# Performance work log

Measured on AMD Instinct MI355X. Metric: run time of the kernel, lower is better.

The kernel has to match this reference:

```python
import jax, jax.numpy as jnp
import numpy as np

B, T, P, D, L = 16, 120, 96, 128, 2


def setup_inputs() -> dict:
    key = jax.random.key(0)
    k1, k2, k3, k4 = jax.random.split(key, 4)
    x = jax.random.normal(k1, (B, P, D, T), dtype=jnp.float32)
    # distances: symmetric-ish positive pairwise distances from random 3D points
    pts = jax.random.uniform(k2, (B, T, P, 3), dtype=jnp.float32) * 5.0
    diff = pts[:, :, :, None, :] - pts[:, :, None, :, :]
    distances = jnp.sqrt(jnp.sum(diff * diff, axis=-1) + 1e-12)
    # contiguous-prefix padding mask (matches the original self-loop loop semantics)
    counts = jax.random.randint(k3, (B,), P // 2, P + 1)
    padding_mask = jnp.arange(P)[None, :] < counts[:, None]
    # params: xavier_uniform with gain 1e-5 ~ tiny; bias 0; LN gamma=1, beta=0
    limit = 1e-5 * np.sqrt(6.0 / (D + D))
    W = jax.random.uniform(k4, (L, D, D), minval=-limit, maxval=limit, dtype=jnp.float32)
    b = jnp.zeros((L, D), dtype=jnp.float32)
    gamma = jnp.ones((L, D), dtype=jnp.float32)
    beta = jnp.zeros((L, D), dtype=jnp.float32)
    return {"x": x, "distances": distances, "padding_mask": padding_mask,
            "W": W, "b": b, "gamma": gamma, "beta": beta}


def _build_adjacency(distances, padding_mask):
    # valid_mask: [B,T,P,P]
    vm2d = (padding_mask[:, :, None] & padding_mask[:, None, :]).astype(distances.dtype)  # [B,P,P]
    vm = vm2d[:, None, :, :]
    vd = distances * vm
    pos = (vd > 0).astype(distances.dtype)
    n = jnp.sum(pos)
    mean = jnp.sum(vd * pos) / n
    var = jnp.sum(((vd - mean) ** 2) * pos) / (n - 1.0)  # unbiased, as torch.std
    sigma = jnp.sqrt(var) + 1e-8
    adj = jnp.exp(-(distances ** 2) / (2.0 * sigma ** 2)) * vm
    # self loops on valid (contiguous-prefix) nodes: add diag(mask)
    eye_mask = jnp.eye(P, dtype=distances.dtype)[None, :, :] * padding_mask[:, :, None].astype(distances.dtype)
    adj = adj + eye_mask[:, None, :, :]
    # symmetric normalization D^{-1/2} A D^{-1/2}
    deg = jnp.clip(jnp.sum(adj, axis=-1, keepdims=True), 1e-8, None)  # [B,T,P,1]
    deg = jnp.clip(deg * padding_mask[:, None, :, None].astype(distances.dtype), 1e-8, None)
    dis = deg ** -0.5
    adj = dis * adj * jnp.swapaxes(dis, -2, -1)
    return adj * vm


def _layer_norm_D(x, g, bt, eps=1e-5):
    # x: [B,P,D,T]; normalize over D axis
    mu = jnp.mean(x, axis=2, keepdims=True)
    var = jnp.mean((x - mu) ** 2, axis=2, keepdims=True)
    return (x - mu) * jax.lax.rsqrt(var + eps) * g[None, None, :, None] + bt[None, None, :, None]


def reference(x, distances, padding_mask, W, b, gamma, beta):
    adj = _build_adjacency(distances, padding_mask)  # [B,T,P,P]
    mask_f = padding_mask.astype(x.dtype)
    for l in range(L):
        xt = jnp.transpose(x, (0, 3, 1, 2))                      # [B,T,P,D]
        h = jnp.einsum('btpd,de->btpe', xt, W[l])                # x @ W
        o = jnp.einsum('btpq,btqd->btpd', adj, h)                # A @ xW
        o = jax.nn.relu(o + b[l])
        o = o * mask_f[:, None, :, None]
        o = jnp.transpose(o, (0, 2, 3, 1))                       # [B,P,D,T]
        o = _layer_norm_D(o, gamma[l], beta[l])
        x = x + o
    return x
```

## Files before the change

### kernel.cpp

```cpp
#include <hip/hip_runtime.h>
#include <math.h>

typedef __bf16 bf16_t;
typedef __bf16 bf16x8 __attribute__((ext_vector_type(8)));
typedef __bf16 bf16x4 __attribute__((ext_vector_type(4)));
typedef float f32x4 __attribute__((ext_vector_type(4)));

namespace {
constexpr int kB = 16;
constexpr int kT = 120;
constexpr int kP = 96;
constexpr int kD = 128;
constexpr int kBT = kB * kT;
constexpr int kPP = kP * kP;
constexpr int kPD = kP * kD;
constexpr long long kND = (long long)kBT * kPP;

constexpr int YS = 136;
constexpr int HS = 104;
constexpr int OS = 132;
constexpr int AS = 104;
constexpr int UNION_B = 26624;
constexpr int AL_OFF = UNION_B;
constexpr int MROW_OFF = AL_OFF + 19968;
constexpr int SMEM_B = MROW_OFF + 384;
}

__device__ __forceinline__ f32x4 mfma16(bf16x8 a, bf16x8 b, f32x4 c) {
    return __builtin_amdgcn_mfma_f32_16x16x32_bf16(a, b, c, 0, 0, 0);
}

__global__ void k_mask(const unsigned char* __restrict__ mraw, int* __restrict__ mask,
                       double* __restrict__ stats) {
    int tid = threadIdx.x;
    if (tid < 4) stats[tid] = 0.0;
    const unsigned int* u32 = (const unsigned int*)mraw;
    unsigned int w0 = u32[0];
    int mode;
    if (w0 == 0x01010101u) mode = 0;
    else if (w0 == 1u) mode = 1;
    else mode = 2;
    for (int i = tid; i < kB * kP; i += blockDim.x) {
        int v;
        if (mode == 0)      v = (mraw[i] != 0);
        else if (mode == 1) v = (u32[i] != 0);
        else                v = (((const float*)mraw)[i] != 0.0f);
        mask[i] = v;
    }
}

__global__ void k_prep(const float* __restrict__ W, bf16_t* __restrict__ wT) {
    int l = blockIdx.y;
    int idx = blockIdx.x * 256 + threadIdx.x;
    int n = idx >> 7, k = idx & 127;
    wT[l * 16384 + n * 128 + k] = (bf16_t)W[l * 16384 + k * 128 + n];
}

__global__ __launch_bounds__(256) void k_stats(const float* __restrict__ dist,
                                               const int* __restrict__ mask,
                                               double* __restrict__ stats) {
    __shared__ int ml[kB * kP];
    for (int i = threadIdx.x; i < kB * kP; i += 256) ml[i] = mask[i];
    __syncthreads();

    long long n4 = kND / 4;
    long long stride = (long long)gridDim.x * 256;
    double s = 0.0, s2 = 0.0;
    int cnt = 0;
    for (long long i4 = (long long)blockIdx.x * 256 + threadIdx.x; i4 < n4; i4 += stride) {
        int q0 = 4 * (int)(i4 % 24);
        long long r = i4 / 24;
        int p = (int)(r % 96);
        int b = (int)((r / 96) / kT);
        const int* mb = ml + b * kP;
        if (mb[p]) {
            float4 d4 = *(const float4*)(dist + i4 * 4);
            if (mb[q0 + 0]) { s += d4.x; s2 += (double)d4.x * d4.x; cnt++; }
            if (mb[q0 + 1]) { s += d4.y; s2 += (double)d4.y * d4.y; cnt++; }
            if (mb[q0 + 2]) { s += d4.z; s2 += (double)d4.z * d4.z; cnt++; }
            if (mb[q0 + 3]) { s += d4.w; s2 += (double)d4.w * d4.w; cnt++; }
        }
    }
    __shared__ double sh[256];
    int tid = threadIdx.x;
    sh[tid] = s; __syncthreads();
    for (int off = 128; off > 0; off >>= 1) { if (tid < off) sh[tid] += sh[tid + off]; __syncthreads(); }
    if (tid == 0) atomicAdd(&stats[0], sh[0]);
    __syncthreads();
    sh[tid] = s2; __syncthreads();
    for (int off = 128; off > 0; off >>= 1) { if (tid < off) sh[tid] += sh[tid + off]; __syncthreads(); }
    if (tid == 0) atomicAdd(&stats[1], sh[0]);
    __syncthreads();
    sh[tid] = (double)cnt; __syncthreads();
    for (int off = 128; off > 0; off >>= 1) { if (tid < off) sh[tid] += sh[tid + off]; __syncthreads(); }
    if (tid == 0) atomicAdd(&stats[2], sh[0]);
}

__global__ void k_fin(const double* __restrict__ stats, float* __restrict__ params) {
    double n = stats[2];
    double mean = stats[0] / n;
    double var = (stats[1] - n * mean * mean) / (n - 1.0);
    double sigma = sqrt(var) + 1e-8;
    params[0] = (float)(1.0 / (2.0 * sigma * sigma));
}

__global__ __launch_bounds__(256) void k_adj(const float* __restrict__ dist,
                                             const int* __restrict__ mask,
                                             const float* __restrict__ params,
                                             bf16_t* __restrict__ adj) {
    __shared__ float aT[kP * 100];
    __shared__ float dis[kP];
    __shared__ float mr[kP];
    int bt = blockIdx.x;
    int b = bt / kT;
    int tid = threadIdx.x;
    if (tid < kP) mr[tid] = (float)mask[b * kP + tid];
    float inv2s2 = params[0];
    __syncthreads();
    const float* dbt = dist + (long long)bt * kPP;
    #pragma unroll
    for (int k = 0; k < 9; ++k) {
        int i4 = k * 256 + tid;
        int e = i4 * 4;
        int p = e / kP, q = e - p * kP;
        float4 d4 = *(const float4*)(dbt + e);
        float mp = mr[p];
        float v[4];
        v[0] = mp * mr[q + 0] != 0.f ? __expf(-d4.x * d4.x * inv2s2) : 0.f;
        v[1] = mp * mr[q + 1] != 0.f ? __expf(-d4.y * d4.y * inv2s2) : 0.f;
        v[2] = mp * mr[q + 2] != 0.f ? __expf(-d4.z * d4.z * inv2s2) : 0.f;
        v[3] = mp * mr[q + 3] != 0.f ? __expf(-d4.w * d4.w * inv2s2) : 0.f;
        #pragma unroll
        for (int j = 0; j < 4; ++j) {
            if (p == q + j) v[j] += mp;
            aT[p * 100 + q + j] = v[j];
        }
    }
    __syncthreads();
    if (tid < kP) {
        float s = 0.f;
        for (int q = 0; q < kP; ++q) s += aT[q * 100 + tid];
        s = fmaxf(s, 1e-8f);
        s = fmaxf(s * mr[tid], 1e-8f);
        dis[tid] = rsqrtf(s);
    }
    __syncthreads();
    bf16_t* obt = adj + (long long)bt * kPP;
    #pragma unroll
    for (int k = 0; k < 9; ++k) {
        int i4 = k * 256 + tid;
        int e = i4 * 4;
        int p = e / kP, q = e - p * kP;
        float dp = dis[p];
        bf16x4 ov;
        #pragma unroll
        for (int j = 0; j < 4; ++j)
            ov[j] = (bf16_t)(dp * aT[p * 100 + q + j] * dis[q + j]);
        *(bf16x4*)(obt + e) = ov;
    }
}

__global__ __launch_bounds__(256) void k_tin(const float* __restrict__ x,
                                             bf16_t* __restrict__ y) {
    __shared__ float tile[64 * 121];
    int b = blockIdx.y, pd0 = blockIdx.x * 64;
    int tid = threadIdx.x;
    const float* xb = x + ((long long)b * kPD + pd0) * kT;
    #pragma unroll
    for (int k = 0; k < 8; ++k) {
        int idx = k * 256 + tid;
        if (idx < 1920) {
            int r = idx / 30, c = idx - r * 30;
            float4 v = *(const float4*)(xb + r * kT + c * 4);
            tile[r * 121 + c * 4 + 0] = v.x;
            tile[r * 121 + c * 4 + 1] = v.y;
            tile[r * 121 + c * 4 + 2] = v.z;
            tile[r * 121 + c * 4 + 3] = v.w;
        }
    }
    __syncthreads();
    bf16_t* yb = y + (long long)b * kT * kPD + pd0;
    #pragma unroll
    for (int k = 0; k < 4; ++k) {
        int idx = k * 256 + tid;
        if (idx < 960) {
            int t = idx >> 3, dg = idx & 7;
            bf16x8 o;
            #pragma unroll
            for (int j = 0; j < 8; ++j) o[j] = (bf16_t)tile[(dg * 8 + j) * 121 + t];
            *(bf16x8*)(yb + (long long)t * kPD + dg * 8) = o;
        }
    }
}

__global__ __launch_bounds__(256) void k_tout(const bf16_t* __restrict__ y,
                                              float* __restrict__ out) {
    __shared__ float tile[64 * 121];
    int b = blockIdx.y, pd0 = blockIdx.x * 64;
    int tid = threadIdx.x;
    const bf16_t* yb = y + (long long)b * kT * kPD + pd0;
    #pragma unroll
    for (int k = 0; k < 4; ++k) {
        int idx = k * 256 + tid;
        if (idx < 960) {
            int t = idx >> 3, dg = idx & 7;
            bf16x8 v = *(const bf16x8*)(yb + (long long)t * kPD + dg * 8);
            #pragma unroll
            for (int j = 0; j < 8; ++j) tile[(dg * 8 + j) * 121 + t] = (float)v[j];
        }
    }
    __syncthreads();
    float* ob = out + ((long long)b * kPD + pd0) * kT;
    #pragma unroll
    for (int k = 0; k < 8; ++k) {
        int idx = k * 256 + tid;
        if (idx < 1920) {
            int r = idx / 30, c = idx - r * 30;
            float4 v;
            v.x = tile[r * 121 + c * 4 + 0];
            v.y = tile[r * 121 + c * 4 + 1];
            v.z = tile[r * 121 + c * 4 + 2];
            v.w = tile[r * 121 + c * 4 + 3];
            *(float4*)(ob + r * kT + c * 4) = v;
        }
    }
}

__global__ __launch_bounds__(512, 5) void k_gcn(bf16_t* __restrict__ y,
                                                const bf16_t* __restrict__ adj,
                                                const int* __restrict__ mask,
                                                const bf16_t* __restrict__ wT,
                                                const float* __restrict__ bias,
                                                const float* __restrict__ gamma,
                                                const float* __restrict__ beta) {
    __shared__ __align__(16) char smem[SMEM_B];
    bf16_t* yL  = (bf16_t*)smem;
    bf16_t* hT  = (bf16_t*)smem;
    bf16_t* oLb = (bf16_t*)smem;
    bf16_t* aL  = (bf16_t*)(smem + AL_OFF);
    float* mrowf = (float*)(smem + MROW_OFF);

    const int tid = threadIdx.x;
    const int tx = tid & 15, ty = tid >> 4;
    const int lane = tid & 63, w = tid >> 6;
    const int wm = w >> 2, wn = w & 3;
    const int fc = lane & 15, fg = lane >> 4;
    const int bt = blockIdx.x, b = bt / kT;
    const int d0 = tx * 8;

    bf16_t* ybt = y + (size_t)bt * kPD;
    const bf16_t* abt = adj + (size_t)bt * kPP;

    if (tid < kP) mrowf[tid] = (float)mask[b * kP + tid];

    #pragma unroll
    for (int k = 0; k < 5; ++k) {
        int i4 = k * 512 + tid;
        if (i4 < 2304) {
            int e4 = i4 * 4;
            int p = e4 / kP, q = e4 - p * kP;
            *(bf16x4*)(aL + p * AS + q) = *(const bf16x4*)(abt + e4);
        }
    }

    bf16x8 yR[3];
    #pragma unroll
    for (int i = 0; i < 3; ++i) {
        int p = ty * 3 + i;
        yR[i] = *(const bf16x8*)(ybt + p * kD + d0);
        *(bf16x8*)(yL + p * YS + d0) = yR[i];
    }

    for (int l = 0; l < 2; ++l) {
        const bf16_t* wTl = wT + l * kD * kD;
        bf16x8 wf[4][2];
        #pragma unroll
        for (int kt = 0; kt < 4; ++kt) {
            wf[kt][0] = *(const bf16x8*)(wTl + ((wn * 2 + 0) * 16 + fc) * kD + kt * 32 + fg * 8);
            wf[kt][1] = *(const bf16x8*)(wTl + ((wn * 2 + 1) * 16 + fc) * kD + kt * 32 + fg * 8);
        }
        __syncthreads();

        f32x4 acc[3][2];
        #pragma unroll
        for (int mt = 0; mt < 3; ++mt) { acc[mt][0] = {0,0,0,0}; acc[mt][1] = {0,0,0,0}; }
        #pragma unroll
        for (int kt = 0; kt < 4; ++kt) {
            #pragma unroll
            for (int mt = 0; mt < 3; ++mt) {
                bf16x8 af = *(const bf16x8*)(yL + ((wm * 3 + mt) * 16 + fc) * YS + kt * 32 + fg * 8);
                acc[mt][0] = mfma16(af, wf[kt][0], acc[mt][0]);
                acc[mt][1] = mfma16(af, wf[kt][1], acc[mt][1]);
            }
        }
        __syncthreads();

        #pragma unroll
        for (int mt = 0; mt < 3; ++mt)
            #pragma unroll
            for (int nn = 0; nn < 2; ++nn) {
                int e = (wn * 2 + nn) * 16 + fc;
                int p0 = (wm * 3 + mt) * 16 + fg * 4;
                bf16x4 hv = {(bf16_t)acc[mt][nn][0], (bf16_t)acc[mt][nn][1],
                             (bf16_t)acc[mt][nn][2], (bf16_t)acc[mt][nn][3]};
                *(bf16x4*)(hT + e * HS + p0) = hv;
            }
        __syncthreads();

        f32x4 acc2[3][2];
        #pragma unroll
        for (int mt = 0; mt < 3; ++mt) { acc2[mt][0] = {0,0,0,0}; acc2[mt][1] = {0,0,0,0}; }
        #pragma unroll
        for (int kt = 0; kt < 3; ++kt) {
            bf16x8 bf0 = *(const bf16x8*)(hT + ((wn * 2 + 0) * 16 + fc) * HS + kt * 32 + fg * 8);
            bf16x8 bf1 = *(const bf16x8*)(hT + ((wn * 2 + 1) * 16 + fc) * HS + kt * 32 + fg * 8);
            #pragma unroll
            for (int mt = 0; mt < 3; ++mt) {
                bf16x8 af = *(const bf16x8*)(aL + ((wm * 3 + mt) * 16 + fc) * AS + kt * 32 + fg * 8);
                acc2[mt][0] = mfma16(af, bf0, acc2[mt][0]);
                acc2[mt][1] = mfma16(af, bf1, acc2[mt][1]);
            }
        }
        __syncthreads();

        #pragma unroll
        for (int mt = 0; mt < 3; ++mt)
            #pragma unroll
            for (int nn = 0; nn < 2; ++nn) {
                int d = (wn * 2 + nn) * 16 + fc;
                int p0 = (wm * 3 + mt) * 16 + fg * 4;
                oLb[(p0 + 0) * OS + d] = (bf16_t)acc2[mt][nn][0];
                oLb[(p0 + 1) * OS + d] = (bf16_t)acc2[mt][nn][1];
                oLb[(p0 + 2) * OS + d] = (bf16_t)acc2[mt][nn][2];
                oLb[(p0 + 3) * OS + d] = (bf16_t)acc2[mt][nn][3];
            }
        __syncthreads();

        const float* bl = bias + l * kD;
        const float* gl = gamma + l * kD;
        const float* bel = beta + l * kD;
        float4 bb0 = *(const float4*)(bl + d0), bb1 = *(const float4*)(bl + d0 + 4);
        float4 gg0 = *(const float4*)(gl + d0), gg1 = *(const float4*)(gl + d0 + 4);
        float4 be0 = *(const float4*)(bel + d0), be1 = *(const float4*)(bel + d0 + 4);
        float bb[8] = {bb0.x, bb0.y, bb0.z, bb0.w, bb1.x, bb1.y, bb1.z, bb1.w};
        float gg[8] = {gg0.x, gg0.y, gg0.z, gg0.w, gg1.x, gg1.y, gg1.z, gg1.w};
        float be[8] = {be0.x, be0.y, be0.z, be0.w, be1.x, be1.y, be1.z, be1.w};

        #pragma unroll
        for (int i = 0; i < 3; ++i) {
            int p = ty * 3 + i;
            float mpf = mrowf[p];
            bf16x4 o0 = *(const bf16x4*)(oLb + p * OS + d0);
            bf16x4 o1 = *(const bf16x4*)(oLb + p * OS + d0 + 4);
            float v[8];
            #pragma unroll
            for (int j = 0; j < 4; ++j) {
                v[j]     = fmaxf((float)o0[j] + bb[j], 0.f) * mpf;
                v[j + 4] = fmaxf((float)o1[j] + bb[j + 4], 0.f) * mpf;
            }
            float s = v[0] + v[1] + v[2] + v[3] + v[4] + v[5] + v[6] + v[7];
            s += __shfl_xor(s, 8);
            s += __shfl_xor(s, 4);
            s += __shfl_xor(s, 2);
            s += __shfl_xor(s, 1);
            float mu = s * 0.0078125f;

            float ss = 0.f;
            #pragma unroll
            for (int j = 0; j < 8; ++j) { float dv = v[j] - mu; ss += dv * dv; }
            ss += __shfl_xor(ss, 8);
            ss += __shfl_xor(ss, 4);
            ss += __shfl_xor(ss, 2);
            ss += __shfl_xor(ss, 1);
            float inv = rsqrtf(ss * 0.0078125f + 1e-5f);

            bf16x8 c;
            #pragma unroll
            for (int j = 0; j < 8; ++j)
                c[j] = (bf16_t)((float)yR[i][j] + (v[j] - mu) * inv * gg[j] + be[j]);
            yR[i] = c;
        }

        if (l == 0) {
            __syncthreads();
            #pragma unroll
            for (int i = 0; i < 3; ++i)
                *(bf16x8*)(yL + (ty * 3 + i) * YS + d0) = yR[i];
        } else {
            #pragma unroll
            for (int i = 0; i < 3; ++i)
                *(bf16x8*)(ybt + (ty * 3 + i) * kD + d0) = yR[i];
        }
    }
}

extern "C" void kernel_launch(void* const* d_in, const int* in_sizes, int n_in,
                              void* d_out, int out_size, void* d_ws, size_t ws_size,
                              hipStream_t stream) {
    (void)in_sizes; (void)n_in; (void)out_size; (void)ws_size;

    const float* x = (const float*)d_in[0];
    const float* dist = (const float*)d_in[1];
    const unsigned char* mraw = (const unsigned char*)d_in[2];
    const float* W = (const float*)d_in[3];
    const float* bias = (const float*)d_in[4];
    const float* gamma = (const float*)d_in[5];
    const float* beta = (const float*)d_in[6];
    float* out = (float*)d_out;

    char* ws = (char*)d_ws;
    double* stats = (double*)ws;
    float* params = (float*)(ws + 32);
    int* mask = (int*)(ws + 64);
    bf16_t* wT = (bf16_t*)(ws + 8192);
    bf16_t* adj = (bf16_t*)(ws + 81920);
    bf16_t* y = (bf16_t*)(ws + 81920 + (size_t)kBT * kPP * 2);

    k_mask<<<1, 256, 0, stream>>>(mraw, mask, stats);
    k_prep<<<dim3(64, 2), 256, 0, stream>>>(W, wT);
    k_stats<<<1024, 256, 0, stream>>>(dist, mask, stats);
    k_fin<<<1, 1, 0, stream>>>(stats, params);
    k_adj<<<kBT, 256, 0, stream>>>(dist, mask, params, adj);

    k_tin<<<dim3(kPD / 64, kB), 256, 0, stream>>>(x, y);

    k_gcn<<<kBT, 512, 0, stream>>>(y, adj, mask, wT, bias, gamma, beta);

    k_tout<<<dim3(kPD / 64, kB), 256, 0, stream>>>(y, out);
}
```

Before: 212.3 us.

## Fuse adjacency construction into GCN kernel and merge mask/prep launches

Adjacency normalization is now computed inside the GCN kernel from raw distances. This removes the bf16 adjacency write and re-read through global memory, along with the separate k_adj and k_fin launches. The mask kernel is merged into the weight-transpose kernel to cut another launch, and y is kept in LDS rather than registers. In exchange, shared memory grows to about 73KB and the launch bounds drop to 2 blocks per CU, which lowers occupancy and adds the exp and normalization work to the GCN critical path.

```diff
diff --git a/kernel.cpp b/kernel.cpp
--- a/kernel.cpp
+++ b/kernel.cpp
@@ -20,40 +20,43 @@
 constexpr int HS = 104;
 constexpr int OS = 132;
 constexpr int AS = 104;
-constexpr int UNION_B = 26624;
-constexpr int AL_OFF = UNION_B;
-constexpr int MROW_OFF = AL_OFF + 19968;
-constexpr int SMEM_B = MROW_OFF + 384;
+constexpr int HT_OFF = 26112;
+constexpr int AL_OFF = 52736;
+constexpr int MROW_OFF = 72704;
+constexpr int DIS_OFF = 73088;
+constexpr int SMEM_B = 73472;
 }
 
 __device__ __forceinline__ f32x4 mfma16(bf16x8 a, bf16x8 b, f32x4 c) {
     return __builtin_amdgcn_mfma_f32_16x16x32_bf16(a, b, c, 0, 0, 0);
 }
 
-__global__ void k_mask(const unsigned char* __restrict__ mraw, int* __restrict__ mask,
+__global__ void k_prep(const float* __restrict__ W, bf16_t* __restrict__ wT,
+                       const unsigned char* __restrict__ mraw, int* __restrict__ mask,
                        double* __restrict__ stats) {
-    int tid = threadIdx.x;
-    if (tid < 4) stats[tid] = 0.0;
-    const unsigned int* u32 = (const unsigned int*)mraw;
-    unsigned int w0 = u32[0];
-    int mode;
-    if (w0 == 0x01010101u) mode = 0;
-    else if (w0 == 1u) mode = 1;
-    else mode = 2;
-    for (int i = tid; i < kB * kP; i += blockDim.x) {
-        int v;
-        if (mode == 0)      v = (mraw[i] != 0);
-        else if (mode == 1) v = (u32[i] != 0);
-        else                v = (((const float*)mraw)[i] != 0.0f);
-        mask[i] = v;
-    }
-}
-
-__global__ void k_prep(const float* __restrict__ W, bf16_t* __restrict__ wT) {
-    int l = blockIdx.y;
-    int idx = blockIdx.x * 256 + threadIdx.x;
+    int bid = blockIdx.x;
+    int l = bid >> 6;
+    int idx = (bid & 63) * 256 + threadIdx.x;
     int n = idx >> 7, k = idx & 127;
     wT[l * 16384 + n * 128 + k] = (bf16_t)W[l * 16384 + k * 128 + n];
+
+    if (bid == 0) {
+        int tid = threadIdx.x;
+        if (tid < 4) stats[tid] = 0.0;
+        const unsigned int* u32 = (const unsigned int*)mraw;
+        unsigned int w0 = u32[0];
+        int mode;
+        if (w0 == 0x01010101u) mode = 0;
+        else if (w0 == 1u) mode = 1;
+        else mode = 2;
+        for (int i = tid; i < kB * kP; i += 256) {
+            int v;
+            if (mode == 0)      v = (mraw[i] != 0);
+            else if (mode == 1) v = (u32[i] != 0);
+            else                v = (((const float*)mraw)[i] != 0.0f);
+            mask[i] = v;
+        }
+    }
 }
 
 __global__ __launch_bounds__(256) void k_stats(const float* __restrict__ dist,
@@ -96,70 +99,6 @@
     if (tid == 0) atomicAdd(&stats[2], sh[0]);
 }
 
-__global__ void k_fin(const double* __restrict__ stats, float* __restrict__ params) {
-    double n = stats[2];
-    double mean = stats[0] / n;
-    double var = (stats[1] - n * mean * mean) / (n - 1.0);
-    double sigma = sqrt(var) + 1e-8;
-    params[0] = (float)(1.0 / (2.0 * sigma * sigma));
-}
-
-__global__ __launch_bounds__(256) void k_adj(const float* __restrict__ dist,
-                                             const int* __restrict__ mask,
-                                             const float* __restrict__ params,
-                                             bf16_t* __restrict__ adj) {
-    __shared__ float aT[kP * 100];
-    __shared__ float dis[kP];
-    __shared__ float mr[kP];
-    int bt = blockIdx.x;
-    int b = bt / kT;
-    int tid = threadIdx.x;
-    if (tid < kP) mr[tid] = (float)mask[b * kP + tid];
-    float inv2s2 = params[0];
-    __syncthreads();
-    const float* dbt = dist + (long long)bt * kPP;
-    #pragma unroll
-    for (int k = 0; k < 9; ++k) {
-        int i4 = k * 256 + tid;
-        int e = i4 * 4;
-        int p = e / kP, q = e - p * kP;
-        float4 d4 = *(const float4*)(dbt + e);
-        float mp = mr[p];
-        float v[4];
-        v[0] = mp * mr[q + 0] != 0.f ? __expf(-d4.x * d4.x * inv2s2) : 0.f;
-        v[1] = mp * mr[q + 1] != 0.f ? __expf(-d4.y * d4.y * inv2s2) : 0.f;
-        v[2] = mp * mr[q + 2] != 0.f ? __expf(-d4.z * d4.z * inv2s2) : 0.f;
-        v[3] = mp * mr[q + 3] != 0.f ? __expf(-d4.w * d4.w * inv2s2) : 0.f;
-        #pragma unroll
-        for (int j = 0; j < 4; ++j) {
-            if (p == q + j) v[j] += mp;
-            aT[p * 100 + q + j] = v[j];
-        }
-    }
-    __syncthreads();
-    if (tid < kP) {
-        float s = 0.f;
-        for (int q = 0; q < kP; ++q) s += aT[q * 100 + tid];
-        s = fmaxf(s, 1e-8f);
-        s = fmaxf(s * mr[tid], 1e-8f);
-        dis[tid] = rsqrtf(s);
-    }
-    __syncthreads();
-    bf16_t* obt = adj + (long long)bt * kPP;
-    #pragma unroll
-    for (int k = 0; k < 9; ++k) {
-        int i4 = k * 256 + tid;
-        int e = i4 * 4;
-        int p = e / kP, q = e - p * kP;
-        float dp = dis[p];
-        bf16x4 ov;
-        #pragma unroll
-        for (int j = 0; j < 4; ++j)
-            ov[j] = (bf16_t)(dp * aT[p * 100 + q + j] * dis[q + j]);
-        *(bf16x4*)(obt + e) = ov;
-    }
-}
-
 __global__ __launch_bounds__(256) void k_tin(const float* __restrict__ x,
                                              bf16_t* __restrict__ y) {
     __shared__ float tile[64 * 121];
@@ -226,19 +165,22 @@
     }
 }
 
-__global__ __launch_bounds__(512, 5) void k_gcn(bf16_t* __restrict__ y,
-                                                const bf16_t* __restrict__ adj,
+__global__ __launch_bounds__(512, 2) void k_gcn(bf16_t* __restrict__ y,
+                                                const float* __restrict__ dist,
                                                 const int* __restrict__ mask,
+                                                const double* __restrict__ stats,
                                                 const bf16_t* __restrict__ wT,
                                                 const float* __restrict__ bias,
                                                 const float* __restrict__ gamma,
                                                 const float* __restrict__ beta) {
     __shared__ __align__(16) char smem[SMEM_B];
     bf16_t* yL  = (bf16_t*)smem;
-    bf16_t* hT  = (bf16_t*)smem;
-    bf16_t* oLb = (bf16_t*)smem;
+    bf16_t* hT  = (bf16_t*)(smem + HT_OFF);
+    bf16_t* oLb = (bf16_t*)(smem + HT_OFF);
+    float*  aT  = (float*)smem;
     bf16_t* aL  = (bf16_t*)(smem + AL_OFF);
     float* mrowf = (float*)(smem + MROW_OFF);
+    float* dis   = (float*)(smem + DIS_OFF);
 
     const int tid = threadIdx.x;
     const int tx = tid & 15, ty = tid >> 4;
@@ -249,26 +191,69 @@
     const int d0 = tx * 8;
 
     bf16_t* ybt = y + (size_t)bt * kPD;
-    const bf16_t* abt = adj + (size_t)bt * kPP;
+    const float* dbt = dist + (size_t)bt * kPP;
 
     if (tid < kP) mrowf[tid] = (float)mask[b * kP + tid];
+
+    double sn = stats[2];
+    double mean = stats[0] / sn;
+    double var = (stats[1] - sn * mean * mean) / (sn - 1.0);
+    double sg = sqrt(var) + 1e-8;
+    float inv2s2 = (float)(1.0 / (2.0 * sg * sg));
+
+    __syncthreads();
 
     #pragma unroll
     for (int k = 0; k < 5; ++k) {
         int i4 = k * 512 + tid;
         if (i4 < 2304) {
-            int e4 = i4 * 4;
-            int p = e4 / kP, q = e4 - p * kP;
-            *(bf16x4*)(aL + p * AS + q) = *(const bf16x4*)(abt + e4);
-        }
-    }
-
-    bf16x8 yR[3];
+            int e = i4 * 4;
+            int p = e / kP, q = e - p * kP;
+            float4 d4 = *(const float4*)(dbt + e);
+            float mp = mrowf[p];
+            float vv[4];
+            vv[0] = (mp * mrowf[q + 0] != 0.f) ? __expf(-d4.x * d4.x * inv2s2) : 0.f;
+            vv[1] = (mp * mrowf[q + 1] != 0.f) ? __expf(-d4.y * d4.y * inv2s2) : 0.f;
+            vv[2] = (mp * mrowf[q + 2] != 0.f) ? __expf(-d4.z * d4.z * inv2s2) : 0.f;
+            vv[3] = (mp * mrowf[q + 3] != 0.f) ? __expf(-d4.w * d4.w * inv2s2) : 0.f;
+            #pragma unroll
+            for (int j = 0; j < 4; ++j) {
+                if (p == q + j) vv[j] += mp;
+                aT[p * 100 + q + j] = vv[j];
+            }
+        }
+    }
+    __syncthreads();
+
+    if (tid < kP) {
+        float s = 0.f;
+        for (int q = 0; q < kP; ++q) s += aT[q * 100 + tid];
+        s = fmaxf(s, 1e-8f);
+        s = fmaxf(s * mrowf[tid], 1e-8f);
+        dis[tid] = rsqrtf(s);
+    }
+    __syncthreads();
+
+    #pragma unroll
+    for (int k = 0; k < 5; ++k) {
+        int i4 = k * 512 + tid;
+        if (i4 < 2304) {
+            int e = i4 * 4;
+            int p = e / kP, q = e - p * kP;
+            float dp = dis[p];
+            bf16x4 ov;
+            #pragma unroll
+            for (int j = 0; j < 4; ++j)
+                ov[j] = (bf16_t)(dp * aT[p * 100 + q + j] * dis[q + j]);
+            *(bf16x4*)(aL + p * AS + q) = ov;
+        }
+    }
+    __syncthreads();
+
     #pragma unroll
     for (int i = 0; i < 3; ++i) {
         int p = ty * 3 + i;
-        yR[i] = *(const bf16x8*)(ybt + p * kD + d0);
-        *(bf16x8*)(yL + p * YS + d0) = yR[i];
+        *(bf16x8*)(yL + p * YS + d0) = *(const bf16x8*)(ybt + p * kD + d0);
     }
 
     for (int l = 0; l < 2; ++l) {
@@ -293,8 +278,6 @@
                 acc[mt][1] = mfma16(af, wf[kt][1], acc[mt][1]);
             }
         }
-        __syncthreads();
-
         #pragma unroll
         for (int mt = 0; mt < 3; ++mt)
             #pragma unroll
@@ -352,6 +335,7 @@
             float mpf = mrowf[p];
             bf16x4 o0 = *(const bf16x4*)(oLb + p * OS + d0);
             bf16x4 o1 = *(const bf16x4*)(oLb + p * OS + d0 + 4);
+            bf16x8 yv = *(const bf16x8*)(yL + p * YS + d0);
             float v[8];
             #pragma unroll
             for (int j = 0; j < 4; ++j) {
@@ -377,19 +361,13 @@
             bf16x8 c;
             #pragma unroll
             for (int j = 0; j < 8; ++j)
-                c[j] = (bf16_t)((float)yR[i][j] + (v[j] - mu) * inv * gg[j] + be[j]);
-            yR[i] = c;
-        }
-
-        if (l == 0) {
-            __syncthreads();
-            #pragma unroll
-            for (int i = 0; i < 3; ++i)
-                *(bf16x8*)(yL + (ty * 3 + i) * YS + d0) = yR[i];
-        } else {
-            #pragma unroll
-            for (int i = 0; i < 3; ++i)
-                *(bf16x8*)(ybt + (ty * 3 + i) * kD + d0) = yR[i];
+                c[j] = (bf16_t)((float)yv[j] + (v[j] - mu) * inv * gg[j] + be[j]);
+
+            if (l == 0) {
+                *(bf16x8*)(yL + p * YS + d0) = c;
+            } else {
+                *(bf16x8*)(ybt + p * kD + d0) = c;
+            }
         }
     }
 }
@@ -410,21 +388,16 @@
 
     char* ws = (char*)d_ws;
     double* stats = (double*)ws;
-    float* params = (float*)(ws + 32);
     int* mask = (int*)(ws + 64);
     bf16_t* wT = (bf16_t*)(ws + 8192);
-    bf16_t* adj = (bf16_t*)(ws + 81920);
-    bf16_t* y = (bf16_t*)(ws + 81920 + (size_t)kBT * kPP * 2);
-
-    k_mask<<<1, 256, 0, stream>>>(mraw, mask, stats);
-    k_prep<<<dim3(64, 2), 256, 0, stream>>>(W, wT);
+    bf16_t* y = (bf16_t*)(ws + 81920);
+
+    k_prep<<<128, 256, 0, stream>>>(W, wT, mraw, mask, stats);
     k_stats<<<1024, 256, 0, stream>>>(dist, mask, stats);
-    k_fin<<<1, 1, 0, stream>>>(stats, params);
-    k_adj<<<kBT, 256, 0, stream>>>(dist, mask, params, adj);
 
     k_tin<<<dim3(kPD / 64, kB), 256, 0, stream>>>(x, y);
 
-    k_gcn<<<kBT, 512, 0, stream>>>(y, adj, mask, wT, bias, gamma, beta);
+    k_gcn<<<kBT, 512, 0, stream>>>(y, dist, mask, stats, wT, bias, gamma, beta);
 
     k_tout<<<dim3(kPD / 64, kB), 256, 0, stream>>>(y, out);
 }
```

After: 183.9 us. 13.4% less time.
